# Kernel tuning notes

Measured on AMD Instinct MI355X. Metric: run time of the kernel, lower is better.

The kernel has to match this reference:

```python
import jax, jax.numpy as jnp
import numpy as np

N_NODES = 100000


def setup_inputs() -> dict:
    key = jax.random.key(0)
    k1, k2, k3, k4 = jax.random.split(key, 4)
    E = 1600000
    D_IN, D_OUT = 128, 128
    feat = jax.random.normal(k1, (N_NODES, D_IN), dtype=jnp.float32)
    src = jax.random.randint(k2, (E,), 0, N_NODES, dtype=jnp.int32)
    dst = jax.random.randint(k3, (E,), 0, N_NODES, dtype=jnp.int32)
    # xavier_uniform for weight [in, out]
    limit = float(np.sqrt(6.0 / (D_IN + D_OUT)))
    weight = jax.random.uniform(k4, (D_IN, D_OUT), dtype=jnp.float32,
                                minval=-limit, maxval=limit)
    bias = jnp.zeros((D_OUT,), dtype=jnp.float32)
    return {"feat": feat, "weight": weight, "bias": bias, "src": src, "dst": dst}


def reference(feat, weight, bias, src, dst):
    # in-degree normalization: norm_i = 1/sqrt(in_deg(i)); clamp deg>=1 to avoid inf
    deg = jax.ops.segment_sum(jnp.ones(src.shape[0], dtype=jnp.float32), dst,
                              num_segments=N_NODES)
    norm = jax.lax.rsqrt(jnp.maximum(deg, 1.0))[:, None]  # [N,1]
    h = feat * norm
    # update_all(copy_src, sum): scatter-sum src features into dst nodes (SpMM)
    agg = jax.ops.segment_sum(h[src], dst, num_segments=N_NODES)  # [N, D_in]
    # in_feats == out_feats -> aggregate first, then dense transform
    rst = agg @ weight          # [N, D_out]
    rst = rst * norm + bias
    return rst
```

## Files before the change

kernel.cpp:

```cpp
#include <hip/hip_runtime.h>


constexpr int N_NODES = 100000;
constexpr int D = 128;
constexpr int NB = 256;
constexpr int GROUP = (N_NODES + NB - 1) / NB;
constexpr int CAP = 14336;

typedef float f32x4 __attribute__((ext_vector_type(4)));
typedef short short8 __attribute__((ext_vector_type(8)));
typedef unsigned uint4v __attribute__((ext_vector_type(4)));

__device__ __forceinline__ ushort f2bf(float x) {
    unsigned u = __float_as_uint(x);
    return (ushort)((u + 0x7fffu + ((u >> 16) & 1u)) >> 16);
}
__device__ __forceinline__ float bf2f(ushort h) {
    return __uint_as_float(((unsigned)h) << 16);
}

__global__ __launch_bounds__(256) void p1_histo(const int* __restrict__ dst, int E,
                                                int* __restrict__ bhist,
                                                const float* __restrict__ W,
                                                ushort* __restrict__ whi,
                                                ushort* __restrict__ wlo) {
    __shared__ int h[NB];
    int t = threadIdx.x, blk = blockIdx.x;
    h[t] = 0;
    if (blk < 64) {
        int p = blk * 256 + t;
        int i  = p & 7;
        int l  = (p >> 3) & 63;
        int kt = (p >> 9) & 3;
        int ct = (p >> 11);
        int k = kt * 32 + (l >> 4) * 8 + i;
        int n = ct * 16 + (l & 15);
        float x = W[k * 128 + n];
        ushort hh = f2bf(x);
        whi[p] = hh;
        wlo[p] = f2bf(x - bf2f(hh));
    }
    __syncthreads();
    int per = (E + NB - 1) / NB;
    int s = blk * per, e = min(E, s + per);
    for (int i = s + t; i < e; i += 256) atomicAdd(&h[dst[i] / GROUP], 1);
    __syncthreads();
    bhist[t * NB + blk] = h[t];
}

__global__ __launch_bounds__(256) void p1_scanrow(int* __restrict__ bhist,
                                                  int* __restrict__ rowtot) {
    __shared__ int lds[256];
    int b = blockIdx.x, t = threadIdx.x;
    int v = bhist[b * NB + t];
    lds[t] = v; __syncthreads();
    for (int off = 1; off < 256; off <<= 1) {
        int x = (t >= off) ? lds[t - off] : 0;
        __syncthreads();
        lds[t] += x;
        __syncthreads();
    }
    bhist[b * NB + t] = lds[t] - v;
    if (t == 255) rowtot[b] = lds[255];
}

__global__ __launch_bounds__(256) void p1_scatter(const int* __restrict__ src,
                                                  const int* __restrict__ dst, int E,
                                                  const int* __restrict__ bhist,
                                                  const int* __restrict__ rowtot,
                                                  int* __restrict__ pairs) {
    __shared__ int loff[NB];
    __shared__ int bb[NB];
    int t = threadIdx.x, blk = blockIdx.x;
    int rv = rowtot[t];
    bb[t] = rv; __syncthreads();
    for (int off = 1; off < 256; off <<= 1) {
        int x = (t >= off) ? bb[t - off] : 0;
        __syncthreads();
        bb[t] += x;
        __syncthreads();
    }
    loff[t] = bhist[t * NB + blk] + bb[t] - rv;
    __syncthreads();
    int per = (E + NB - 1) / NB;
    int s = blk * per, e = min(E, s + per);
    for (int i = s + t; i < e; i += 256) {
        int d = dst[i];
        int b = d / GROUP;
        int pos = atomicAdd(&loff[b], 1);
        pairs[pos] = ((d - b * GROUP) << 17) | src[i];
    }
}

__global__ __launch_bounds__(256) void p2_all(const int* __restrict__ pairs,
                                              const int* __restrict__ rowtot,
                                              int* __restrict__ deg,
                                              int* __restrict__ offs,
                                              float* __restrict__ norm,
                                              int* __restrict__ esrc) {
    __shared__ int h[512];
    __shared__ int ssum[256];
    __shared__ int bb[256];
    __shared__ int sbuf[CAP];
    int t = threadIdx.x, b = blockIdx.x;
    int lo = b * GROUP;
    int cnt = min(GROUP, N_NODES - lo);

    int rv = rowtot[t];
    bb[t] = rv;
    h[t] = 0; h[t + 256] = 0;
    __syncthreads();
    for (int off = 1; off < 256; off <<= 1) {
        int x = (t >= off) ? bb[t - off] : 0;
        __syncthreads();
        bb[t] += x;
        __syncthreads();
    }
    int s1 = bb[b];
    int s0 = s1 - rowtot[b];
    __syncthreads();

    for (int i = s0 + t; i < s1; i += 256) atomicAdd(&h[pairs[i] >> 17], 1);
    __syncthreads();

    int v0 = h[2 * t], v1 = h[2 * t + 1];
    int s = v0 + v1;
    ssum[t] = s; __syncthreads();
    for (int off = 1; off < 256; off <<= 1) {
        int x = (t >= off) ? ssum[t - off] : 0;
        __syncthreads();
        ssum[t] += x;
        __syncthreads();
    }
    int pre = ssum[t] - s;
    if (2 * t < cnt) {
        int node = lo + 2 * t;
        deg[node] = v0;
        offs[node] = s0 + pre;
        norm[node] = rsqrtf(fmaxf((float)v0, 1.0f));
    }
    if (2 * t + 1 < cnt) {
        int node = lo + 2 * t + 1;
        deg[node] = v1;
        offs[node] = s0 + pre + v0;
        norm[node] = rsqrtf(fmaxf((float)v1, 1.0f));
    }
    __syncthreads();
    h[2 * t] = pre;
    h[2 * t + 1] = pre + v0;
    __syncthreads();

    int wsize = s1 - s0;
    bool fits = (wsize <= CAP);
    for (int i = s0 + t; i < s1; i += 256) {
        int p = pairs[i];
        int dl = p >> 17;
        int sv = p & 0x1FFFF;
        int pos = atomicAdd(&h[dl], 1);
        if (fits) sbuf[pos] = sv; else esrc[s0 + pos] = sv;
    }
    __syncthreads();
    if (fits)
        for (int i = t; i < wsize; i += 256) esrc[s0 + i] = sbuf[i];
}

__global__ void k_featbf(const float* __restrict__ feat, const float* __restrict__ norm,
                         uint2* __restrict__ ft2, int total) {
    int i = blockIdx.x * blockDim.x + threadIdx.x;
    if (i < total) {
        float w = norm[i >> 5];
        f32x4 v = ((const f32x4*)feat)[i];
        uint2 o;
        o.x = (unsigned)f2bf(v[0] * w) | ((unsigned)f2bf(v[1] * w) << 16);
        o.y = (unsigned)f2bf(v[2] * w) | ((unsigned)f2bf(v[3] * w) << 16);
        ft2[i] = o;
    }
}

__global__ __launch_bounds__(256) void k_gather16(const unsigned* __restrict__ ft,
                                                  const int* __restrict__ offs,
                                                  const int* __restrict__ deg,
                                                  const int* __restrict__ esrc,
                                                  unsigned* __restrict__ outbf) {
    int gtid = blockIdx.x * blockDim.x + threadIdx.x;
    int node = gtid >> 6;
    if (node >= N_NODES) return;
    int lane = gtid & 63;
    int g  = lane >> 4;
    int sl = lane & 15;
    int start = offs[node];
    int cnt   = deg[node];
    int last  = start + cnt - 1;
    float acc[8] = {0.f, 0.f, 0.f, 0.f, 0.f, 0.f, 0.f, 0.f};
    const uint4v* ftv = (const uint4v*)ft;
    for (int j = 0; j < cnt; j += 16) {
        int i0 = start + j + g;
        int s0v = esrc[min(i0,      last)];
        int s1v = esrc[min(i0 + 4,  last)];
        int s2v = esrc[min(i0 + 8,  last)];
        int s3v = esrc[min(i0 + 12, last)];
        float w0 = (j + g      < cnt) ? 1.0f : 0.0f;
        float w1 = (j + g + 4  < cnt) ? 1.0f : 0.0f;
        float w2 = (j + g + 8  < cnt) ? 1.0f : 0.0f;
        float w3 = (j + g + 12 < cnt) ? 1.0f : 0.0f;
        uint4v u0 = ftv[(size_t)s0v * 16 + sl];
        uint4v u1 = ftv[(size_t)s1v * 16 + sl];
        uint4v u2 = ftv[(size_t)s2v * 16 + sl];
        uint4v u3 = ftv[(size_t)s3v * 16 + sl];
        #pragma unroll
        for (int q = 0; q < 4; ++q) {
            unsigned a = u0[q];
            acc[q * 2]     = fmaf(__uint_as_float(a << 16),         w0, acc[q * 2]);
            acc[q * 2 + 1] = fmaf(__uint_as_float(a & 0xffff0000u), w0, acc[q * 2 + 1]);
        }
        #pragma unroll
        for (int q = 0; q < 4; ++q) {
            unsigned a = u1[q];
            acc[q * 2]     = fmaf(__uint_as_float(a << 16),         w1, acc[q * 2]);
            acc[q * 2 + 1] = fmaf(__uint_as_float(a & 0xffff0000u), w1, acc[q * 2 + 1]);
        }
        #pragma unroll
        for (int q = 0; q < 4; ++q) {
            unsigned a = u2[q];
            acc[q * 2]     = fmaf(__uint_as_float(a << 16),         w2, acc[q * 2]);
            acc[q * 2 + 1] = fmaf(__uint_as_float(a & 0xffff0000u), w2, acc[q * 2 + 1]);
        }
        #pragma unroll
        for (int q = 0; q < 4; ++q) {
            unsigned a = u3[q];
            acc[q * 2]     = fmaf(__uint_as_float(a << 16),         w3, acc[q * 2]);
            acc[q * 2 + 1] = fmaf(__uint_as_float(a & 0xffff0000u), w3, acc[q * 2 + 1]);
        }
    }
    #pragma unroll
    for (int q = 0; q < 8; ++q) {
        acc[q] += __shfl_xor(acc[q], 16, 64);
        acc[q] += __shfl_xor(acc[q], 32, 64);
    }
    if (g == 0) {
        uint4v o;
        #pragma unroll
        for (int q = 0; q < 4; ++q)
            o[q] = (unsigned)f2bf(acc[q * 2]) | ((unsigned)f2bf(acc[q * 2 + 1]) << 16);
        ((uint4v*)outbf)[(size_t)node * 16 + sl] = o;
    }
}

__global__ __launch_bounds__(256) void k_gemm_bf(const ushort* __restrict__ aggbf,
                                                 const ushort* __restrict__ whi,
                                                 const ushort* __restrict__ wlo,
                                                 const float* __restrict__ bias,
                                                 const float* __restrict__ norm,
                                                 float* __restrict__ out) {
    __shared__ ushort sH[16384];
    __shared__ ushort sL[16384];
    {
        const short8* gh = (const short8*)whi;
        const short8* gl = (const short8*)wlo;
        short8* lh = (short8*)sH;
        short8* ll = (short8*)sL;
        for (int i = threadIdx.x; i < 2048; i += 256) { lh[i] = gh[i]; ll[i] = gl[i]; }
    }
    __syncthreads();

    const int lane = threadIdx.x & 63;
    const int wid  = threadIdx.x >> 6;
    const int rsub = lane & 15;
    const int kgrp = lane >> 4;

    const short8* BH = (const short8*)sH;
    const short8* BL = (const short8*)sL;

    const int nstrips = N_NODES / 16;
    for (int strip = blockIdx.x * 4 + wid; strip < nstrips; strip += gridDim.x * 4) {
        const int row0 = strip * 16;
        const ushort* arow = aggbf + (size_t)(row0 + rsub) * D + kgrp * 8;
        short8 a[4];
        #pragma unroll
        for (int kt = 0; kt < 4; ++kt) a[kt] = *(const short8*)(arow + kt * 32);
        float nr[4];
        #pragma unroll
        for (int r = 0; r < 4; ++r) nr[r] = norm[row0 + kgrp * 4 + r];

        #pragma unroll
        for (int ct = 0; ct < 8; ++ct) {
            f32x4 acc = {0.f, 0.f, 0.f, 0.f};
            #pragma unroll
            for (int kt = 0; kt < 4; ++kt) {
                acc = __builtin_amdgcn_mfma_f32_16x16x32_bf16(a[kt], BH[(ct * 4 + kt) * 64 + lane], acc, 0, 0, 0);
                acc = __builtin_amdgcn_mfma_f32_16x16x32_bf16(a[kt], BL[(ct * 4 + kt) * 64 + lane], acc, 0, 0, 0);
            }
            const float bc = bias[ct * 16 + rsub];
            float* ocol = out + (size_t)row0 * D + ct * 16 + rsub;
            #pragma unroll
            for (int r = 0; r < 4; ++r) {
                int row = kgrp * 4 + r;
                ocol[(size_t)row * D] = acc[r] * nr[r] + bc;
            }
        }
    }
}

__global__ void k_scatter(const float* __restrict__ feat, const int* __restrict__ src,
                          const int* __restrict__ dst, const float* __restrict__ norm,
                          int E, float* __restrict__ agg) {
    long long gtid = (long long)blockIdx.x * blockDim.x + threadIdx.x;
    int e    = (int)(gtid >> 6);
    int lane = (int)(gtid & 63);
    if (e >= E) return;
    int s = src[e];
    int t = dst[e];
    float ns = norm[s];
    float2 v = ((const float2*)(feat + (size_t)s * D))[lane];
    float* arow = agg + (size_t)t * D + lane * 2;
    atomicAdd(arow + 0, v.x * ns);
    atomicAdd(arow + 1, v.y * ns);
}
__global__ void k_deg_f(const int* __restrict__ dst, int E, float* __restrict__ deg) {
    int i = blockIdx.x * blockDim.x + threadIdx.x;
    if (i < E) atomicAdd(deg + dst[i], 1.0f);
}
__global__ void k_norm_f(float* __restrict__ dn) {
    int i = blockIdx.x * blockDim.x + threadIdx.x;
    if (i < N_NODES) dn[i] = rsqrtf(fmaxf(dn[i], 1.0f));
}
__global__ __launch_bounds__(256) void k_gemm(float* __restrict__ io,
                                              const float* __restrict__ W,
                                              const float* __restrict__ bias,
                                              const float* __restrict__ norm) {
    __shared__ float sW[D * D];
    __shared__ float srow[2][D];
    for (int i = threadIdx.x; i < D * D; i += 256) sW[i] = W[i];
    const int r = threadIdx.x >> 7;
    const int c = threadIdx.x & 127;
    const float bc = bias[c];
    const int npairs = N_NODES / 2;
    for (int rp = blockIdx.x; rp < npairs; rp += gridDim.x) {
        __syncthreads();
        const int row = rp * 2 + r;
        srow[r][c] = io[(size_t)row * D + c];
        __syncthreads();
        float acc = 0.f;
        #pragma unroll 8
        for (int k = 0; k < D; ++k)
            acc = fmaf(srow[r][k], sW[k * D + c], acc);
        io[(size_t)row * D + c] = acc * norm[row] + bc;
    }
}

extern "C" void kernel_launch(void* const* d_in, const int* in_sizes, int n_in,
                              void* d_out, int out_size, void* d_ws, size_t ws_size,
                              hipStream_t stream) {
    const float* feat   = (const float*)d_in[0];
    const float* weight = (const float*)d_in[1];
    const float* bias   = (const float*)d_in[2];
    const int*   src    = (const int*)d_in[3];
    const int*   dst    = (const int*)d_in[4];
    const int E = in_sizes[3];

    int* pairs = (int*)d_out;

    uintptr_t cur = (uintptr_t)d_ws;
    auto take = [&](size_t bytes) -> void* {
        uintptr_t r = (cur + 63) & ~(uintptr_t)63;
        cur = r + bytes;
        return (void*)r;
    };

    size_t S_ft  = (size_t)N_NODES * 64 * 4;
    size_t S_agg = (size_t)N_NODES * D * 2;
    size_t need  = S_ft + S_agg +
                   (size_t)(3 * N_NODES + 256 + NB * NB + E) * 4 + 65536 + 1024;

    unsigned* ft     = (unsigned*)take(S_ft);
    ushort*   aggbf  = (ushort*)take(S_agg);
    float*    norm   = (float*)take((size_t)N_NODES * 4);
    int*      deg    = (int*)take((size_t)N_NODES * 4);
    int*      offs   = (int*)take((size_t)N_NODES * 4);
    int*      rowtot = (int*)take(256 * 4);
    int*      bhist  = (int*)take((size_t)NB * NB * 4);
    int*      esrc   = (int*)take((size_t)E * 4);
    ushort*   whi    = (ushort*)take(16384 * 2);
    ushort*   wlo    = (ushort*)take(16384 * 2);

    if (ws_size >= need) {
        p1_histo<<<NB, 256, 0, stream>>>(dst, E, bhist, weight, whi, wlo);
        p1_scanrow<<<NB, 256, 0, stream>>>(bhist, rowtot);
        p1_scatter<<<NB, 256, 0, stream>>>(src, dst, E, bhist, rowtot, pairs);
        p2_all<<<NB, 256, 0, stream>>>(pairs, rowtot, deg, offs, norm, esrc);
        k_featbf<<<(N_NODES * 32 + 255) / 256, 256, 0, stream>>>(feat, norm, (uint2*)ft, N_NODES * 32);
        long long gthreads = (long long)N_NODES * 64;
        k_gather16<<<(int)((gthreads + 255) / 256), 256, 0, stream>>>(ft, offs, deg, esrc, (unsigned*)aggbf);
        k_gemm_bf<<<1024, 256, 0, stream>>>(aggbf, whi, wlo, bias, norm, (float*)d_out);
    } else {
        float* agg = (float*)d_out;
        hipMemsetAsync(d_out, 0, (size_t)N_NODES * D * sizeof(float), stream);
        hipMemsetAsync(norm, 0, (size_t)N_NODES * sizeof(float), stream);
        k_deg_f<<<(E + 255) / 256, 256, 0, stream>>>(dst, E, (float*)norm);
        k_norm_f<<<(N_NODES + 255) / 256, 256, 0, stream>>>((float*)norm);
        long long sthreads = (long long)E * 64;
        k_scatter<<<(int)((sthreads + 255) / 256), 256, 0, stream>>>(feat, src, dst, (float*)norm, E, agg);
        k_gemm<<<4096, 256, 0, stream>>>(agg, weight, bias, (float*)norm);
    }
}
```

Before: 139.3 us.

## Fuse neighbor gather with bf16 MFMA GEMM via per-wave LDS strip

Merges the gather-aggregate kernel and the GEMM kernel into one. Each wave now aggregates 16 consecutive nodes sequentially into a padded LDS tile, then runs the MFMA transform straight from LDS. This removes the bf16 aggregate round trip through global memory and one launch. In exchange, each wave handles 16 nodes serially instead of one node per wave, which cuts gather parallelism and latency hiding. The weight fragments are now read from global memory/L2 rather than being staged in LDS.

Measured after the change: 150.3 us. 1.08x slower.

```diff
diff --git a/kernel.cpp b/kernel.cpp
--- a/kernel.cpp
+++ b/kernel.cpp
@@ -6,6 +6,7 @@
 constexpr int NB = 256;
 constexpr int GROUP = (N_NODES + NB - 1) / NB;
 constexpr int CAP = 14336;
+constexpr int RPAD = 136;
 
 typedef float f32x4 __attribute__((ext_vector_type(4)));
 typedef short short8 __attribute__((ext_vector_type(8)));
@@ -177,111 +178,100 @@
     }
 }
 
-__global__ __launch_bounds__(256) void k_gather16(const unsigned* __restrict__ ft,
-                                                  const int* __restrict__ offs,
-                                                  const int* __restrict__ deg,
-                                                  const int* __restrict__ esrc,
-                                                  unsigned* __restrict__ outbf) {
-    int gtid = blockIdx.x * blockDim.x + threadIdx.x;
-    int node = gtid >> 6;
-    if (node >= N_NODES) return;
-    int lane = gtid & 63;
-    int g  = lane >> 4;
-    int sl = lane & 15;
-    int start = offs[node];
-    int cnt   = deg[node];
-    int last  = start + cnt - 1;
-    float acc[8] = {0.f, 0.f, 0.f, 0.f, 0.f, 0.f, 0.f, 0.f};
+__global__ __launch_bounds__(256) void k_gather_gemm(const unsigned* __restrict__ ft,
+                                                     const int* __restrict__ offs,
+                                                     const int* __restrict__ deg,
+                                                     const int* __restrict__ esrc,
+                                                     const ushort* __restrict__ whi,
+                                                     const ushort* __restrict__ wlo,
+                                                     const float* __restrict__ bias,
+                                                     const float* __restrict__ norm,
+                                                     float* __restrict__ out) {
+    __shared__ ushort sA[4][16 * RPAD];
+    const int wid  = threadIdx.x >> 6;
+    const int lane = threadIdx.x & 63;
+    const int g  = lane >> 4;
+    const int sl = lane & 15;
+    const int strip = blockIdx.x * 4 + wid;
+    const bool active = (strip < N_NODES / 16);
+    const int row0 = strip * 16;
     const uint4v* ftv = (const uint4v*)ft;
-    for (int j = 0; j < cnt; j += 16) {
-        int i0 = start + j + g;
-        int s0v = esrc[min(i0,      last)];
-        int s1v = esrc[min(i0 + 4,  last)];
-        int s2v = esrc[min(i0 + 8,  last)];
-        int s3v = esrc[min(i0 + 12, last)];
-        float w0 = (j + g      < cnt) ? 1.0f : 0.0f;
-        float w1 = (j + g + 4  < cnt) ? 1.0f : 0.0f;
-        float w2 = (j + g + 8  < cnt) ? 1.0f : 0.0f;
-        float w3 = (j + g + 12 < cnt) ? 1.0f : 0.0f;
-        uint4v u0 = ftv[(size_t)s0v * 16 + sl];
-        uint4v u1 = ftv[(size_t)s1v * 16 + sl];
-        uint4v u2 = ftv[(size_t)s2v * 16 + sl];
-        uint4v u3 = ftv[(size_t)s3v * 16 + sl];
-        #pragma unroll
-        for (int q = 0; q < 4; ++q) {
-            unsigned a = u0[q];
-            acc[q * 2]     = fmaf(__uint_as_float(a << 16),         w0, acc[q * 2]);
-            acc[q * 2 + 1] = fmaf(__uint_as_float(a & 0xffff0000u), w0, acc[q * 2 + 1]);
+
+    if (active) {
+        for (int n = 0; n < 16; ++n) {
+            int node = row0 + n;
+            int start = offs[node];
+            int cnt   = deg[node];
+            int last  = start + cnt - 1;
+            float acc[8] = {0.f, 0.f, 0.f, 0.f, 0.f, 0.f, 0.f, 0.f};
+            for (int j = 0; j < cnt; j += 16) {
+                int i0 = start + j + g;
+                int s0v = esrc[min(i0,      last)];
+                int s1v = esrc[min(i0 + 4,  last)];
+                int s2v = esrc[min(i0 + 8,  last)];
+                int s3v = esrc[min(i0 + 12, last)];
+                float w0 = (j + g      < cnt) ? 1.0f : 0.0f;
+                float w1 = (j + g + 4  < cnt) ? 1.0f : 0.0f;
+                float w2 = (j + g + 8  < cnt) ? 1.0f : 0.0f;
+                float w3 = (j + g + 12 < cnt) ? 1.0f : 0.0f;
+                uint4v u0 = ftv[(size_t)s0v * 16 + sl];
+                uint4v u1 = ftv[(size_t)s1v * 16 + sl];
+                uint4v u2 = ftv[(size_t)s2v * 16 + sl];
+                uint4v u3 = ftv[(size_t)s3v * 16 + sl];
+                #pragma unroll
+                for (int q = 0; q < 4; ++q) {
+                    unsigned a = u0[q];
+                    acc[q * 2]     = fmaf(__uint_as_float(a << 16),         w0, acc[q * 2]);
+                    acc[q * 2 + 1] = fmaf(__uint_as_float(a & 0xffff0000u), w0, acc[q * 2 + 1]);
+                }
+                #pragma unroll
+                for (int q = 0; q < 4; ++q) {
+                    unsigned a = u1[q];
+                    acc[q * 2]     = fmaf(__uint_as_float(a << 16),         w1, acc[q * 2]);
+                    acc[q * 2 + 1] = fmaf(__uint_as_float(a & 0xffff0000u), w1, acc[q * 2 + 1]);
+                }
+                #pragma unroll
+                for (int q = 0; q < 4; ++q) {
+                    unsigned a = u2[q];
+                    acc[q * 2]     = fmaf(__uint_as_float(a << 16),         w2, acc[q * 2]);
+                    acc[q * 2 + 1] = fmaf(__uint_as_float(a & 0xffff0000u), w2, acc[q * 2 + 1]);
+                }
+                #pragma unroll
+                for (int q = 0; q < 4; ++q) {
+                    unsigned a = u3[q];
+                    acc[q * 2]     = fmaf(__uint_as_float(a << 16),         w3, acc[q * 2]);
+                    acc[q * 2 + 1] = fmaf(__uint_as_float(a & 0xffff0000u), w3, acc[q * 2 + 1]);
+                }
+            }
+            #pragma unroll
+            for (int q = 0; q < 8; ++q) {
+                acc[q] += __shfl_xor(acc[q], 16, 64);
+                acc[q] += __shfl_xor(acc[q], 32, 64);
+            }
+            if (g == 0) {
+                uint4v o;
+                #pragma unroll
+                for (int q = 0; q < 4; ++q)
+                    o[q] = (unsigned)f2bf(acc[q * 2]) | ((unsigned)f2bf(acc[q * 2 + 1]) << 16);
+                *(uint4v*)(&sA[wid][n * RPAD + sl * 8]) = o;
+            }
         }
-        #pragma unroll
-        for (int q = 0; q < 4; ++q) {
-            unsigned a = u1[q];
-            acc[q * 2]     = fmaf(__uint_as_float(a << 16),         w1, acc[q * 2]);
-            acc[q * 2 + 1] = fmaf(__uint_as_float(a & 0xffff0000u), w1, acc[q * 2 + 1]);
-        }
-        #pragma unroll
-        for (int q = 0; q < 4; ++q) {
-            unsigned a = u2[q];
-            acc[q * 2]     = fmaf(__uint_as_float(a << 16),         w2, acc[q * 2]);
-            acc[q * 2 + 1] = fmaf(__uint_as_float(a & 0xffff0000u), w2, acc[q * 2 + 1]);
-        }
-        #pragma unroll
-        for (int q = 0; q < 4; ++q) {
-            unsigned a = u3[q];
-            acc[q * 2]     = fmaf(__uint_as_float(a << 16),         w3, acc[q * 2]);
-            acc[q * 2 + 1] = fmaf(__uint_as_float(a & 0xffff0000u), w3, acc[q * 2 + 1]);
-        }
-    }
-    #pragma unroll
-    for (int q = 0; q < 8; ++q) {
-        acc[q] += __shfl_xor(acc[q], 16, 64);
-        acc[q] += __shfl_xor(acc[q], 32, 64);
-    }
-    if (g == 0) {
-        uint4v o;
-        #pragma unroll
-        for (int q = 0; q < 4; ++q)
-            o[q] = (unsigned)f2bf(acc[q * 2]) | ((unsigned)f2bf(acc[q * 2 + 1]) << 16);
-        ((uint4v*)outbf)[(size_t)node * 16 + sl] = o;
-    }
-}
-
-__global__ __launch_bounds__(256) void k_gemm_bf(const ushort* __restrict__ aggbf,
-                                                 const ushort* __restrict__ whi,
-                                                 const ushort* __restrict__ wlo,
-                                                 const float* __restrict__ bias,
-                                                 const float* __restrict__ norm,
-                                                 float* __restrict__ out) {
-    __shared__ ushort sH[16384];
-    __shared__ ushort sL[16384];
-    {
-        const short8* gh = (const short8*)whi;
-        const short8* gl = (const short8*)wlo;
-        short8* lh = (short8*)sH;
-        short8* ll = (short8*)sL;
-        for (int i = threadIdx.x; i < 2048; i += 256) { lh[i] = gh[i]; ll[i] = gl[i]; }
-    }
-    __syncthreads();
-
-    const int lane = threadIdx.x & 63;
-    const int wid  = threadIdx.x >> 6;
-    const int rsub = lane & 15;
-    const int kgrp = lane >> 4;
-
-    const short8* BH = (const short8*)sH;
-    const short8* BL = (const short8*)sL;
-
-    const int nstrips = N_NODES / 16;
-    for (int strip = blockIdx.x * 4 + wid; strip < nstrips; strip += gridDim.x * 4) {
-        const int row0 = strip * 16;
-        const ushort* arow = aggbf + (size_t)(row0 + rsub) * D + kgrp * 8;
+    }
+    __syncthreads();
+
+    if (active) {
+        const int rsub = lane & 15;
+        const int kgrp = lane >> 4;
         short8 a[4];
         #pragma unroll
-        for (int kt = 0; kt < 4; ++kt) a[kt] = *(const short8*)(arow + kt * 32);
+        for (int kt = 0; kt < 4; ++kt)
+            a[kt] = *(const short8*)(&sA[wid][rsub * RPAD + kt * 32 + kgrp * 8]);
         float nr[4];
         #pragma unroll
         for (int r = 0; r < 4; ++r) nr[r] = norm[row0 + kgrp * 4 + r];
 
+        const short8* BH = (const short8*)whi;
+        const short8* BL = (const short8*)wlo;
         #pragma unroll
         for (int ct = 0; ct < 8; ++ct) {
             f32x4 acc = {0.f, 0.f, 0.f, 0.f};
@@ -368,12 +358,10 @@
     };
 
     size_t S_ft  = (size_t)N_NODES * 64 * 4;
-    size_t S_agg = (size_t)N_NODES * D * 2;
-    size_t need  = S_ft + S_agg +
+    size_t need  = S_ft +
                    (size_t)(3 * N_NODES + 256 + NB * NB + E) * 4 + 65536 + 1024;
 
     unsigned* ft     = (unsigned*)take(S_ft);
-    ushort*   aggbf  = (ushort*)take(S_agg);
     float*    norm   = (float*)take((size_t)N_NODES * 4);
     int*      deg    = (int*)take((size_t)N_NODES * 4);
     int*      offs   = (int*)take((size_t)N_NODES * 4);
@@ -389,9 +377,10 @@
         p1_scatter<<<NB, 256, 0, stream>>>(src, dst, E, bhist, rowtot, pairs);
         p2_all<<<NB, 256, 0, stream>>>(pairs, rowtot, deg, offs, norm, esrc);
         k_featbf<<<(N_NODES * 32 + 255) / 256, 256, 0, stream>>>(feat, norm, (uint2*)ft, N_NODES * 32);
-        long long gthreads = (long long)N_NODES * 64;
-        k_gather16<<<(int)((gthreads + 255) / 256), 256, 0, stream>>>(ft, offs, deg, esrc, (unsigned*)aggbf);
-        k_gemm_bf<<<1024, 256, 0, stream>>>(aggbf, whi, wlo, bias, norm, (float*)d_out);
+        const int nstrips = N_NODES / 16;
+        k_gather_gemm<<<(nstrips + 3) / 4, 256, 0, stream>>>(ft, offs, deg, esrc,
+                                                             whi, wlo, bias, norm,
+                                                             (float*)d_out);
     } else {
         float* agg = (float*)d_out;
         hipMemsetAsync(d_out, 0, (size_t)N_NODES * D * sizeof(float), stream);
```

## Fold feature bf16 conversion into histogram kernel, apply source norm in gather

Applied to the files above, without the earlier changes.

The feature-to-bf16 conversion no longer depends on the degree norm. It is merged into the first histogram kernel as extra blocks that run alongside the dst histogram, which removes a separate launch and lets the conversion overlap with the binning. The per-source norm is now applied inside the gather as a per-edge weight loaded from norm[src]. This adds one scattered scalar load per edge and changes rounding slightly, since bf16 now quantizes the unscaled features.

Result: no change. 139.0 us (-0.2%).

```diff
diff --git a/kernel.cpp b/kernel.cpp
--- a/kernel.cpp
+++ b/kernel.cpp
@@ -6,6 +6,7 @@
 constexpr int NB = 256;
 constexpr int GROUP = (N_NODES + NB - 1) / NB;
 constexpr int CAP = 14336;
+constexpr int CONVB = 1280;
 
 typedef float f32x4 __attribute__((ext_vector_type(4)));
 typedef short short8 __attribute__((ext_vector_type(8)));
@@ -19,13 +20,27 @@
     return __uint_as_float(((unsigned)h) << 16);
 }
 
-__global__ __launch_bounds__(256) void p1_histo(const int* __restrict__ dst, int E,
-                                                int* __restrict__ bhist,
-                                                const float* __restrict__ W,
-                                                ushort* __restrict__ whi,
-                                                ushort* __restrict__ wlo) {
+__global__ __launch_bounds__(256) void p1_histo_conv(const int* __restrict__ dst, int E,
+                                                     int* __restrict__ bhist,
+                                                     const float* __restrict__ W,
+                                                     ushort* __restrict__ whi,
+                                                     ushort* __restrict__ wlo,
+                                                     const float* __restrict__ feat,
+                                                     uint2* __restrict__ ft2) {
+    int t = threadIdx.x, blk = blockIdx.x;
+    if (blk >= NB) {
+        int base = (blk - NB) * 256 + t;
+        int stride = CONVB * 256;
+        for (int i = base; i < N_NODES * 32; i += stride) {
+            f32x4 v = ((const f32x4*)feat)[i];
+            uint2 o;
+            o.x = (unsigned)f2bf(v[0]) | ((unsigned)f2bf(v[1]) << 16);
+            o.y = (unsigned)f2bf(v[2]) | ((unsigned)f2bf(v[3]) << 16);
+            ft2[i] = o;
+        }
+        return;
+    }
     __shared__ int h[NB];
-    int t = threadIdx.x, blk = blockIdx.x;
     h[t] = 0;
     if (blk < 64) {
         int p = blk * 256 + t;
@@ -164,23 +179,11 @@
         for (int i = t; i < wsize; i += 256) esrc[s0 + i] = sbuf[i];
 }
 
-__global__ void k_featbf(const float* __restrict__ feat, const float* __restrict__ norm,
-                         uint2* __restrict__ ft2, int total) {
-    int i = blockIdx.x * blockDim.x + threadIdx.x;
-    if (i < total) {
-        float w = norm[i >> 5];
-        f32x4 v = ((const f32x4*)feat)[i];
-        uint2 o;
-        o.x = (unsigned)f2bf(v[0] * w) | ((unsigned)f2bf(v[1] * w) << 16);
-        o.y = (unsigned)f2bf(v[2] * w) | ((unsigned)f2bf(v[3] * w) << 16);
-        ft2[i] = o;
-    }
-}
-
 __global__ __launch_bounds__(256) void k_gather16(const unsigned* __restrict__ ft,
                                                   const int* __restrict__ offs,
                                                   const int* __restrict__ deg,
                                                   const int* __restrict__ esrc,
+                                                  const float* __restrict__ norm,
                                                   unsigned* __restrict__ outbf) {
     int gtid = blockIdx.x * blockDim.x + threadIdx.x;
     int node = gtid >> 6;
@@ -199,10 +202,10 @@
         int s1v = esrc[min(i0 + 4,  last)];
         int s2v = esrc[min(i0 + 8,  last)];
         int s3v = esrc[min(i0 + 12, last)];
-        float w0 = (j + g      < cnt) ? 1.0f : 0.0f;
-        float w1 = (j + g + 4  < cnt) ? 1.0f : 0.0f;
-        float w2 = (j + g + 8  < cnt) ? 1.0f : 0.0f;
-        float w3 = (j + g + 12 < cnt) ? 1.0f : 0.0f;
+        float w0 = (j + g      < cnt) ? norm[s0v] : 0.0f;
+        float w1 = (j + g + 4  < cnt) ? norm[s1v] : 0.0f;
+        float w2 = (j + g + 8  < cnt) ? norm[s2v] : 0.0f;
+        float w3 = (j + g + 12 < cnt) ? norm[s3v] : 0.0f;
         uint4v u0 = ftv[(size_t)s0v * 16 + sl];
         uint4v u1 = ftv[(size_t)s1v * 16 + sl];
         uint4v u2 = ftv[(size_t)s2v * 16 + sl];
@@ -384,13 +387,14 @@
     ushort*   wlo    = (ushort*)take(16384 * 2);
 
     if (ws_size >= need) {
-        p1_histo<<<NB, 256, 0, stream>>>(dst, E, bhist, weight, whi, wlo);
+        p1_histo_conv<<<NB + CONVB, 256, 0, stream>>>(dst, E, bhist, weight, whi, wlo,
+                                                      feat, (uint2*)ft);
         p1_scanrow<<<NB, 256, 0, stream>>>(bhist, rowtot);
         p1_scatter<<<NB, 256, 0, stream>>>(src, dst, E, bhist, rowtot, pairs);
         p2_all<<<NB, 256, 0, stream>>>(pairs, rowtot, deg, offs, norm, esrc);
-        k_featbf<<<(N_NODES * 32 + 255) / 256, 256, 0, stream>>>(feat, norm, (uint2*)ft, N_NODES * 32);
         long long gthreads = (long long)N_NODES * 64;
-        k_gather16<<<(int)((gthreads + 255) / 256), 256, 0, stream>>>(ft, offs, deg, esrc, (unsigned*)aggbf);
+        k_gather16<<<(int)((gthreads + 255) / 256), 256, 0, stream>>>(ft, offs, deg, esrc,
+                                                                      norm, (unsigned*)aggbf);
         k_gemm_bf<<<1024, 256, 0, stream>>>(aggbf, whi, wlo, bias, norm, (float*)d_out);
     } else {
         float* agg = (float*)d_out;
```
